# Optimization experiments

Measured on AMD Instinct MI355X. Metric: run time of the kernel, lower is better.

The kernel has to match this reference:

```python
import jax, jax.numpy as jnp
import numpy as np

# int64 needed: the torch module hashes with int64 primes (2654435761 > 2**31)
jax.config.update("jax_enable_x64", True)

NUM_LEVELS = 16
BASE_RES = 16
MAX_RES = 2048
LOG2_HASHMAP = 19
FEATURE_DIM = 2
HASHMAP_SIZE = 2 ** LOG2_HASHMAP
N_POINTS = 1_048_576

_growth = np.exp((np.log(MAX_RES) - np.log(BASE_RES)) / (NUM_LEVELS - 1))
RESOLUTIONS = [min(int(BASE_RES * _growth ** l), MAX_RES) for l in range(NUM_LEVELS)]
PRIMES = np.array([1, 2654435761, 805459861], dtype=np.int64)
# corner order matches torch triple loop: index c = i*4 + j*2 + k -> offset [i, j, k]
OFFSETS = np.array([[i, j, k] for i in range(2) for j in range(2) for k in range(2)],
                   dtype=np.int64)  # (8, 3)


def setup_inputs() -> dict:
    key = jax.random.key(0)
    k1, k2 = jax.random.split(key)
    positions = jax.random.uniform(k1, (N_POINTS, 3), dtype=jnp.float32) * 2.0 - 1.0  # in [-1, 1]
    hash_table = jax.random.normal(k2, (HASHMAP_SIZE, FEATURE_DIM), dtype=jnp.float32) * 1e-4
    return {"positions": positions, "hash_table": hash_table}


def _encode(positions, hash_table):
    p = (positions + 1.0) * 0.5  # map [-1,1] -> [0,1]
    primes = jnp.asarray(PRIMES)
    offs = jnp.asarray(OFFSETS)           # (8, 3) int64
    offs_f = offs.astype(p.dtype)         # (8, 3)
    feats = []
    for res in RESOLUTIONS:
        sp = p * (res - 1)                # (N, 3)
        gp = jnp.floor(sp)
        w = sp - gp                       # fractional weights (N, 3)
        corners = gp.astype(jnp.int64)[:, None, :] + offs[None]   # (N, 8, 3)
        corners = jnp.clip(corners, 0, res - 1)
        h = (corners[..., 0] * primes[0]) ^ (corners[..., 1] * primes[1]) ^ (corners[..., 2] * primes[2])
        idx = h % HASHMAP_SIZE            # (N, 8)
        cf = hash_table[idx]              # gather: (N, 8, F)
        # trilinear weights: prod over dims of (w if offset bit else 1-w)
        wcomp = offs_f[None] * w[:, None, :] + (1.0 - offs_f[None]) * (1.0 - w[:, None, :])  # (N,8,3)
        tw = wcomp[..., 0] * wcomp[..., 1] * wcomp[..., 2]        # (N, 8)
        feats.append(jnp.einsum('nc,ncf->nf', tw, cf))            # (N, F)
    return jnp.concatenate(feats, axis=-1)  # (N, NUM_LEVELS * F)


def reference(positions, hash_table):
    return _encode(positions, hash_table)
```

## Files before the change

### kernel.cpp

```cpp
#include <hip/hip_runtime.h>
#include <cstdint>

#define P2 2654435761u
#define P3 805459861u
#define HMASK 524287u

__constant__ int RES[16] = {16, 22, 30, 42, 58, 80, 111, 153,
                            212, 294, 406, 561, 776, 1072, 1482, 2048};

__global__ __launch_bounds__(256) void hash_enc_kernel(
    const float* __restrict__ pos, const float2* __restrict__ tbl,
    float2* __restrict__ out, int n)
{
    __shared__ int sres[16];
    if (threadIdx.x < 16) sres[threadIdx.x] = RES[threadIdx.x];
    __syncthreads();

    int t = blockIdx.x * 256 + threadIdx.x;
    int i = t >> 4;
    int l = t & 15;
    if (i >= n) return;

    float x = (pos[3 * i + 0] + 1.0f) * 0.5f;
    float y = (pos[3 * i + 1] + 1.0f) * 0.5f;
    float z = (pos[3 * i + 2] + 1.0f) * 0.5f;

    const int rm1 = sres[l] - 1;
    const float rf = (float)rm1;

    float sx = x * rf, sy = y * rf, sz = z * rf;
    float fx = floorf(sx), fy = floorf(sy), fz = floorf(sz);
    float wx = sx - fx, wy = sy - fy, wz = sz - fz;
    int x0 = (int)fx, y0 = (int)fy, z0 = (int)fz;
    int x0c = min(max(x0, 0), rm1), x1c = min(max(x0 + 1, 0), rm1);
    int y0c = min(max(y0, 0), rm1), y1c = min(max(y0 + 1, 0), rm1);
    int z0c = min(max(z0, 0), rm1), z1c = min(max(z0 + 1, 0), rm1);

    uint32_t hx0 = (uint32_t)x0c,      hx1 = (uint32_t)x1c;
    uint32_t hy0 = (uint32_t)y0c * P2, hy1 = (uint32_t)y1c * P2;
    uint32_t hz0 = (uint32_t)z0c * P3, hz1 = (uint32_t)z1c * P3;

    uint32_t i000 = (hx0 ^ hy0 ^ hz0) & HMASK;
    uint32_t i001 = (hx0 ^ hy0 ^ hz1) & HMASK;
    uint32_t i010 = (hx0 ^ hy1 ^ hz0) & HMASK;
    uint32_t i011 = (hx0 ^ hy1 ^ hz1) & HMASK;
    uint32_t i100 = (hx1 ^ hy0 ^ hz0) & HMASK;
    uint32_t i101 = (hx1 ^ hy0 ^ hz1) & HMASK;
    uint32_t i110 = (hx1 ^ hy1 ^ hz0) & HMASK;
    uint32_t i111 = (hx1 ^ hy1 ^ hz1) & HMASK;

    float2 c000 = tbl[i000];
    float2 c001 = tbl[i001];
    float2 c010 = tbl[i010];
    float2 c011 = tbl[i011];
    float2 c100 = tbl[i100];
    float2 c101 = tbl[i101];
    float2 c110 = tbl[i110];
    float2 c111 = tbl[i111];

    float ux = 1.0f - wx, uy = 1.0f - wy, uz = 1.0f - wz;
    float w00 = ux * uy, w01 = ux * wy, w10 = wx * uy, w11 = wx * wy;
    float f0, f1;
    f0  = (w00 * uz) * c000.x; f1  = (w00 * uz) * c000.y;
    f0 += (w00 * wz) * c001.x; f1 += (w00 * wz) * c001.y;
    f0 += (w01 * uz) * c010.x; f1 += (w01 * uz) * c010.y;
    f0 += (w01 * wz) * c011.x; f1 += (w01 * wz) * c011.y;
    f0 += (w10 * uz) * c100.x; f1 += (w10 * uz) * c100.y;
    f0 += (w10 * wz) * c101.x; f1 += (w10 * wz) * c101.y;
    f0 += (w11 * uz) * c110.x; f1 += (w11 * uz) * c110.y;
    f0 += (w11 * wz) * c111.x; f1 += (w11 * wz) * c111.y;

    out[t] = make_float2(f0, f1);
}

extern "C" void kernel_launch(void* const* d_in, const int* in_sizes, int n_in,
                              void* d_out, int out_size, void* d_ws, size_t ws_size,
                              hipStream_t stream) {
    const float* pos = (const float*)d_in[0];
    const float2* tbl = (const float2*)d_in[1];
    float2* out = (float2*)d_out;
    int n = in_sizes[0] / 3;
    long long total = (long long)n * 16;
    dim3 grid((unsigned)((total + 255) / 256)), block(256);
    hash_enc_kernel<<<grid, block, 0, stream>>>(pos, tbl, out, n);
}
```

Before: 618.1 us.

## Pair x-adjacent hash corners into float4 gathers and stage positions in LDS

When the lower x corner is even, the upper x corner's hash index differs only in bit 0, so both entries sit in one aligned 16-byte slot. The kernel now fetches them with four float4 loads instead of eight float2 loads. Lanes with an odd x corner reload the upper four corners separately, so those lanes diverge and do extra work. Point positions are loaded once per block into shared memory with nontemporal vector loads, and outputs use nontemporal stores. This relies on x1c being x0c+1, which breaks only when clamping makes them equal at an even boundary.

```diff
diff --git a/kernel.cpp b/kernel.cpp
--- a/kernel.cpp
+++ b/kernel.cpp
@@ -4,6 +4,9 @@
 #define P2 2654435761u
 #define P3 805459861u
 #define HMASK 524287u
+
+typedef float nfloat4 __attribute__((ext_vector_type(4)));
+typedef float nfloat2 __attribute__((ext_vector_type(2)));
 
 __constant__ int RES[16] = {16, 22, 30, 42, 58, 80, 111, 153,
                             212, 294, 406, 561, 776, 1072, 1482, 2048};
@@ -12,18 +15,38 @@
     const float* __restrict__ pos, const float2* __restrict__ tbl,
     float2* __restrict__ out, int n)
 {
+    const float4* __restrict__ tbl4 = (const float4*)tbl;
+
     __shared__ int sres[16];
-    if (threadIdx.x < 16) sres[threadIdx.x] = RES[threadIdx.x];
+    __shared__ float spos[48];
+
+    const int tid = threadIdx.x;
+    if (tid < 16) sres[tid] = RES[tid];
+
+    const int p0 = blockIdx.x * 16;
+    if (p0 + 16 <= n) {
+        if (tid < 12) {
+            nfloat4 v = __builtin_nontemporal_load(
+                (const nfloat4*)(pos + (size_t)p0 * 3) + tid);
+            ((nfloat4*)spos)[tid] = v;
+        }
+    } else {
+        if (tid < 48) {
+            int gi = p0 * 3 + tid;
+            spos[tid] = (gi < 3 * n) ? pos[gi] : 0.0f;
+        }
+    }
     __syncthreads();
 
-    int t = blockIdx.x * 256 + threadIdx.x;
-    int i = t >> 4;
-    int l = t & 15;
+    const int t = blockIdx.x * 256 + tid;
+    const int i = t >> 4;
+    const int l = t & 15;
     if (i >= n) return;
+    const int li = tid >> 4;
 
-    float x = (pos[3 * i + 0] + 1.0f) * 0.5f;
-    float y = (pos[3 * i + 1] + 1.0f) * 0.5f;
-    float z = (pos[3 * i + 2] + 1.0f) * 0.5f;
+    float x = (spos[3 * li + 0] + 1.0f) * 0.5f;
+    float y = (spos[3 * li + 1] + 1.0f) * 0.5f;
+    float z = (spos[3 * li + 2] + 1.0f) * 0.5f;
 
     const int rm1 = sres[l] - 1;
     const float rf = (float)rm1;
@@ -36,27 +59,42 @@
     int y0c = min(max(y0, 0), rm1), y1c = min(max(y0 + 1, 0), rm1);
     int z0c = min(max(z0, 0), rm1), z1c = min(max(z0 + 1, 0), rm1);
 
-    uint32_t hx0 = (uint32_t)x0c,      hx1 = (uint32_t)x1c;
     uint32_t hy0 = (uint32_t)y0c * P2, hy1 = (uint32_t)y1c * P2;
     uint32_t hz0 = (uint32_t)z0c * P3, hz1 = (uint32_t)z1c * P3;
+    uint32_t m00 = hy0 ^ hz0;
+    uint32_t m01 = hy0 ^ hz1;
+    uint32_t m10 = hy1 ^ hz0;
+    uint32_t m11 = hy1 ^ hz1;
 
-    uint32_t i000 = (hx0 ^ hy0 ^ hz0) & HMASK;
-    uint32_t i001 = (hx0 ^ hy0 ^ hz1) & HMASK;
-    uint32_t i010 = (hx0 ^ hy1 ^ hz0) & HMASK;
-    uint32_t i011 = (hx0 ^ hy1 ^ hz1) & HMASK;
-    uint32_t i100 = (hx1 ^ hy0 ^ hz0) & HMASK;
-    uint32_t i101 = (hx1 ^ hy0 ^ hz1) & HMASK;
-    uint32_t i110 = (hx1 ^ hy1 ^ hz0) & HMASK;
-    uint32_t i111 = (hx1 ^ hy1 ^ hz1) & HMASK;
+    uint32_t hx0 = (uint32_t)x0c;
+    uint32_t j000 = (hx0 ^ m00) & HMASK;
+    uint32_t j001 = (hx0 ^ m01) & HMASK;
+    uint32_t j010 = (hx0 ^ m10) & HMASK;
+    uint32_t j011 = (hx0 ^ m11) & HMASK;
 
-    float2 c000 = tbl[i000];
-    float2 c001 = tbl[i001];
-    float2 c010 = tbl[i010];
-    float2 c011 = tbl[i011];
-    float2 c100 = tbl[i100];
-    float2 c101 = tbl[i101];
-    float2 c110 = tbl[i110];
-    float2 c111 = tbl[i111];
+    float4 q00 = tbl4[j000 >> 1];
+    float4 q01 = tbl4[j001 >> 1];
+    float4 q10 = tbl4[j010 >> 1];
+    float4 q11 = tbl4[j011 >> 1];
+
+    float2 c000, c001, c010, c011, c100, c101, c110, c111;
+    bool b00 = (j000 & 1), b01 = (j001 & 1), b10 = (j010 & 1), b11 = (j011 & 1);
+    c000 = b00 ? make_float2(q00.z, q00.w) : make_float2(q00.x, q00.y);
+    c100 = b00 ? make_float2(q00.x, q00.y) : make_float2(q00.z, q00.w);
+    c001 = b01 ? make_float2(q01.z, q01.w) : make_float2(q01.x, q01.y);
+    c101 = b01 ? make_float2(q01.x, q01.y) : make_float2(q01.z, q01.w);
+    c010 = b10 ? make_float2(q10.z, q10.w) : make_float2(q10.x, q10.y);
+    c110 = b10 ? make_float2(q10.x, q10.y) : make_float2(q10.z, q10.w);
+    c011 = b11 ? make_float2(q11.z, q11.w) : make_float2(q11.x, q11.y);
+    c111 = b11 ? make_float2(q11.x, q11.y) : make_float2(q11.z, q11.w);
+
+    if (x0c & 1) {
+        uint32_t hx1 = (uint32_t)x1c;
+        c100 = tbl[(hx1 ^ m00) & HMASK];
+        c101 = tbl[(hx1 ^ m01) & HMASK];
+        c110 = tbl[(hx1 ^ m10) & HMASK];
+        c111 = tbl[(hx1 ^ m11) & HMASK];
+    }
 
     float ux = 1.0f - wx, uy = 1.0f - wy, uz = 1.0f - wz;
     float w00 = ux * uy, w01 = ux * wy, w10 = wx * uy, w11 = wx * wy;
@@ -70,7 +108,8 @@
     f0 += (w11 * uz) * c110.x; f1 += (w11 * uz) * c110.y;
     f0 += (w11 * wz) * c111.x; f1 += (w11 * wz) * c111.y;
 
-    out[t] = make_float2(f0, f1);
+    nfloat2 r; r.x = f0; r.y = f1;
+    __builtin_nontemporal_store(r, (nfloat2*)&out[t]);
 }
 
 extern "C" void kernel_launch(void* const* d_in, const int* in_sizes, int n_in,
```

After: 525.6 us. -15.0%, faster.
